# Performance work log

Hardware: AMD Instinct MI355X
Metric: run time of the kernel (lower is better)

The kernel has to match this reference:

```python
import jax, jax.numpy as jnp
import numpy as np

B, P, L, D, H = 32, 256, 64, 128, 8
DH = D // H
NP_, NL, E = B * P, B * L, B * P * L
LN_EPS = 1e-5


def setup_inputs() -> dict:
    key = jax.random.key(0)
    ks = jax.random.split(key, 32)
    def rn(i, shape, scale=0.05):
        return jax.random.normal(ks[i], shape, dtype=jnp.float32) * scale
    # uniform batch layout: graph b owns protein nodes [b*P,(b+1)*P) and ligand nodes [b*L,(b+1)*L)
    pe = (np.arange(B)[:, None] * P + np.repeat(np.arange(P), L)[None, :]).reshape(-1)
    le = (np.arange(B)[:, None] * L + np.tile(np.arange(L), P)[None, :]).reshape(-1)
    return {
        'h_protein': rn(0, (NP_, D), 1.0), 'h_ligand': rn(1, (NL, D), 1.0),
        'p_edge_idx': jnp.asarray(pe, jnp.int32), 'l_edge_idx': jnp.asarray(le, jnp.int32),
        'Wq_l': rn(2, (D, D)), 'Wk_p': rn(3, (D, D)), 'Wv_p': rn(4, (D, D)),
        'Wg_l': rn(5, (2 * D, D)), 'bg_l': jnp.zeros((D,), jnp.float32),
        'Wu_l': rn(6, (D, D)), 'bu_l': jnp.zeros((D,), jnp.float32),
        'Wq_p': rn(7, (D, D)), 'Wk_l': rn(8, (D, D)), 'Wv_l': rn(9, (D, D)),
        'Wg_p': rn(10, (2 * D, D)), 'bg_p': jnp.zeros((D,), jnp.float32),
        'Wu_p': rn(11, (D, D)), 'bu_p': jnp.zeros((D,), jnp.float32),
        'ln_p_g': jnp.ones((D,), jnp.float32), 'ln_p_b': jnp.zeros((D,), jnp.float32),
        'ln_l_g': jnp.ones((D,), jnp.float32), 'ln_l_b': jnp.zeros((D,), jnp.float32),
        'W1_p': rn(12, (D, 4 * D)), 'b1_p': jnp.zeros((4 * D,), jnp.float32),
        'W2_p': rn(13, (4 * D, D)), 'b2_p': jnp.zeros((D,), jnp.float32),
        'W1_l': rn(14, (D, 4 * D)), 'b1_l': jnp.zeros((4 * D,), jnp.float32),
        'W2_l': rn(15, (4 * D, D)), 'b2_l': jnp.zeros((D,), jnp.float32),
    }


def _layernorm(x, g, b):
    mu = jnp.mean(x, axis=-1, keepdims=True)
    var = jnp.mean(jnp.square(x - mu), axis=-1, keepdims=True)
    return (x - mu) * jax.lax.rsqrt(var + LN_EPS) * g + b


def _seg_softmax(scores, seg, n):  # scores [E,H], seg [E]
    m = jax.ops.segment_max(scores, seg, num_segments=n)
    e = jnp.exp(scores - m[seg])
    s = jax.ops.segment_sum(e, seg, num_segments=n)
    return e / s[seg]


def _side(hq, hkv, q_edge, kv_edge, nq, Wq, Wk, Wv, Wg, bg, Wu, bu):
    q = (hq @ Wq).reshape(-1, H, DH)
    k = (hkv @ Wk).reshape(-1, H, DH)
    v = (hkv @ Wv).reshape(-1, H, DH)
    scores = jnp.sum(q[q_edge] * k[kv_edge], axis=-1) / np.sqrt(DH)  # [E,H]
    att = _seg_softmax(scores, q_edge, nq)
    ctx = jax.ops.segment_sum(v[kv_edge] * att[:, :, None], q_edge, num_segments=nq)
    ctx = ctx.reshape(nq, D)
    gate = jax.nn.sigmoid(jnp.concatenate([hq, ctx], axis=1) @ Wg + bg)
    return hq + gate * (ctx @ Wu + bu)


def reference(h_protein, h_ligand, p_edge_idx, l_edge_idx,
              Wq_l, Wk_p, Wv_p, Wg_l, bg_l, Wu_l, bu_l,
              Wq_p, Wk_l, Wv_l, Wg_p, bg_p, Wu_p, bu_p,
              ln_p_g, ln_p_b, ln_l_g, ln_l_b,
              W1_p, b1_p, W2_p, b2_p, W1_l, b1_l, W2_l, b2_l):
    n_p, n_l = h_protein.shape[0], h_ligand.shape[0]
    # ligand attends to protein
    h_l_upd = _side(h_ligand, h_protein, l_edge_idx, p_edge_idx, n_l,
                    Wq_l, Wk_p, Wv_p, Wg_l, bg_l, Wu_l, bu_l)
    # protein attends to ligand
    h_p_upd = _side(h_protein, h_ligand, p_edge_idx, l_edge_idx, n_p,
                    Wq_p, Wk_l, Wv_l, Wg_p, bg_p, Wu_p, bu_p)
    # FFN blocks (dropout = identity in eval mode)
    hp = _layernorm(h_p_upd, ln_p_g, ln_p_b)
    protein_final = h_p_upd + jax.nn.relu(hp @ W1_p + b1_p) @ W2_p + b2_p
    hl = _layernorm(h_l_upd, ln_l_g, ln_l_b)
    ligand_final = h_l_upd + jax.nn.relu(hl @ W1_l + b1_l) @ W2_l + b2_l
    return (protein_final, ligand_final)
```

## Files before the change

### kernel.cpp

```cpp
#include <hip/hip_runtime.h>
#include <hip/hip_bf16.h>

typedef __bf16 bf16x8 __attribute__((ext_vector_type(8)));
typedef __bf16 bf16x4 __attribute__((ext_vector_type(4)));
typedef float  f32x4  __attribute__((ext_vector_type(4)));
typedef unsigned short u16;

#define NPROT 8192
#define NLIG  2048
#define DMODEL 128
#define NHEAD 8
#define NBATCH 32
#define PPB 256
#define LPB 64

__device__ __forceinline__ u16 f2bf(float f){
  union { float f; unsigned int u; } v; v.f = f;
  return (u16)((v.u + 0x7FFFu + ((v.u >> 16) & 1u)) >> 16);
}

__device__ __forceinline__ bf16x8 cvt8(const float* p){
  float4 a = *(const float4*)p, b = *(const float4*)(p + 4);
  bf16x8 r;
  r[0]=(__bf16)a.x; r[1]=(__bf16)a.y; r[2]=(__bf16)a.z; r[3]=(__bf16)a.w;
  r[4]=(__bf16)b.x; r[5]=(__bf16)b.y; r[6]=(__bf16)b.z; r[7]=(__bf16)b.w;
  return r;
}

struct QkvJob { const float* A; const float* Wsrc[3]; u16* outB; int N; int blockStart; };
struct TJob { const float* src; u16* dst; int M, K, tilesX, blockStart; };
struct L1Args {
  QkvJob qjobs[2];
  int nQkv;
  int nprep;
  TJob pjobs[10];
};

__global__ __launch_bounds__(256) void l1_kernel(L1Args a){
  __shared__ u16 Wl[64][136];
  __shared__ u16 Al[64][136];
  __shared__ float tile[32][33];
  int bid = (int)blockIdx.x;
  int tid = (int)threadIdx.x;
  if (bid < a.nQkv){
    int j = (bid >= a.qjobs[1].blockStart) ? 1 : 0;
    const QkvJob jb = a.qjobs[j];
    int t = bid - jb.blockStart;
    int tn = t / 6, tm = t - tn * 6;
    {
      int midx = tm >> 1;
      int cb64 = (tm & 1) * 64;
      const float* Ws = jb.Wsrc[midx];
      int kr = tid >> 2;
      int cb = (tid & 3) * 16;
      #pragma unroll
      for (int p = 0; p < 2; ++p){
        int k = p * 64 + kr;
        const float* srcp = Ws + (size_t)k * 128 + cb64 + cb;
        float4 v0 = *(const float4*)srcp,     v1 = *(const float4*)(srcp + 4);
        float4 v2 = *(const float4*)(srcp+8), v3 = *(const float4*)(srcp + 12);
        float tmp[16] = {v0.x,v0.y,v0.z,v0.w, v1.x,v1.y,v1.z,v1.w,
                         v2.x,v2.y,v2.z,v2.w, v3.x,v3.y,v3.z,v3.w};
        #pragma unroll
        for (int i = 0; i < 16; ++i) Wl[cb + i][k] = f2bf(tmp[i]);
      }
    }
    {
      const float* Asrc = jb.A + (size_t)(tn * 64) * 128;
      #pragma unroll
      for (int p = 0; p < 8; ++p){
        int idx = p * 256 + tid;
        int r = idx >> 5, c4 = (idx & 31) * 4;
        float4 v = *(const float4*)(Asrc + (size_t)r * 128 + c4);
        Al[r][c4+0] = f2bf(v.x); Al[r][c4+1] = f2bf(v.y);
        Al[r][c4+2] = f2bf(v.z); Al[r][c4+3] = f2bf(v.w);
      }
    }
    __syncthreads();
    int w = tid >> 6, l = tid & 63;
    int rloc = (w >> 1) * 32;
    int cloc = (w & 1) * 32;
    int lr = l & 15, lk = (l >> 4) * 8;
    f32x4 a00 = {0.f,0.f,0.f,0.f}, a01 = a00, a10 = a00, a11 = a00;
    #pragma unroll
    for (int kk = 0; kk < 128; kk += 32){
      bf16x8 a0 = *(const bf16x8*)&Al[rloc + lr][kk + lk];
      bf16x8 a1 = *(const bf16x8*)&Al[rloc + 16 + lr][kk + lk];
      bf16x8 b0 = *(const bf16x8*)&Wl[cloc + lr][kk + lk];
      bf16x8 b1 = *(const bf16x8*)&Wl[cloc + 16 + lr][kk + lk];
      a00 = __builtin_amdgcn_mfma_f32_16x16x32_bf16(a0, b0, a00, 0, 0, 0);
      a01 = __builtin_amdgcn_mfma_f32_16x16x32_bf16(a0, b1, a01, 0, 0, 0);
      a10 = __builtin_amdgcn_mfma_f32_16x16x32_bf16(a1, b0, a10, 0, 0, 0);
      a11 = __builtin_amdgcn_mfma_f32_16x16x32_bf16(a1, b1, a11, 0, 0, 0);
    }
    __syncthreads();
    {
      f32x4 av[2][2] = {{a00, a01}, {a10, a11}};
      int lg4 = l >> 4;
      #pragma unroll
      for (int i = 0; i < 2; ++i)
        #pragma unroll
        for (int jj = 0; jj < 2; ++jj)
          #pragma unroll
          for (int e = 0; e < 4; ++e)
            Al[rloc + i * 16 + lg4 * 4 + e][cloc + jj * 16 + lr] = f2bf(av[i][jj][e]);
    }
    __syncthreads();
    {
      int row = tid >> 2;
      int hseg = tid & 3;
      int m = tm >> 1;
      int h = (tm & 1) * 4 + hseg;
      const u16* srcl = &Al[row][hseg * 16];
      u16* dst = jb.outB + ((size_t)m * NHEAD + h) * (size_t)jb.N * 16
                         + (size_t)(tn * 64 + row) * 16;
      *(bf16x8*)dst = *(const bf16x8*)srcl;
      *(bf16x8*)(dst + 8) = *(const bf16x8*)(srcl + 8);
    }
  } else {
    int pb = bid - a.nQkv;
    int j = 0;
    while (j + 1 < a.nprep && pb >= a.pjobs[j + 1].blockStart) ++j;
    const TJob jb = a.pjobs[j];
    int t = pb - jb.blockStart;
    int tm = t % jb.tilesX, tk = t / jb.tilesX;
    int c = tid & 31, r0 = tid >> 5;
    #pragma unroll
    for (int p = 0; p < 4; ++p)
      tile[r0 + p * 8][c] = jb.src[(size_t)(tk * 32 + r0 + p * 8) * jb.M + tm * 32 + c];
    __syncthreads();
    {
      int c2 = tid >> 7;
      int lch = (tid >> 1) & 63;
      int eh = (tid & 1) * 4;
      int kl = (lch >> 4) * 8 + eh;
      int ml = c2 * 16 + (lch & 15);
      ushort4 o;
      o.x = f2bf(tile[kl + 0][ml]);
      o.y = f2bf(tile[kl + 1][ml]);
      o.z = f2bf(tile[kl + 2][ml]);
      o.w = f2bf(tile[kl + 3][ml]);
      size_t off = ((size_t)(tm * 2 + c2) * (jb.K >> 5) + tk) * 512 + lch * 8 + eh;
      *(ushort4*)&jb.dst[off] = o;
    }
  }
}

struct K2Args {
  const u16 *qkv_p, *qkv_l;
  const float *h_f[2];
  const u16 *WgT[2], *WgB[2], *WuT[2];
  const float *bg[2], *bu[2], *lng[2], *lnb[2];
  const u16 *W1T[2], *W2T[2];
  const float *b1[2], *b2[2];
  float* out[2];
};

struct K2B {
  float hu[32 * 132];
  union { float hstg[32 * 132]; u16 t[32 * 520]; } x;
};

__global__ __launch_bounds__(512) void k2_kernel(K2Args args){
  __shared__ __align__(16) union {
    struct { u16 vT[8 * 1152]; u16 P[8 * 2304]; } a;
    K2B b;
  } su;
  __shared__ __align__(16) u16 s_ctx[32 * 128];

  int bid = (int)blockIdx.x;
  int tid = (int)threadIdx.x;
  int w = tid >> 6, l = tid & 63, lr = l & 15, lg4 = l >> 4;
  int lk = lg4 * 8;

  int side, rowbase, batch, NC;
  if (bid < NLIG / 32){ side = 1; rowbase = bid * 32; batch = rowbase >> 6; NC = 4; }
  else { side = 0; rowbase = (bid - NLIG / 32) * 32; batch = rowbase >> 8; NC = 1; }

  int NRs = side == 0 ? NPROT : NLIG;
  int NRo = side == 0 ? NLIG : NPROT;
  int orowoff = side == 0 ? batch * LPB : batch * PPB;
  const u16* qbase = (side == 0 ? args.qkv_p : args.qkv_l);
  const u16* obase = (side == 0 ? args.qkv_l : args.qkv_p);
  const u16* kbase = obase + (size_t)NHEAD * NRo * 16;
  const u16* vbase = obase + (size_t)2 * NHEAD * NRo * 16;

  bf16x8 zero8;
  #pragma unroll
  for (int i = 0; i < 8; ++i) zero8[i] = (__bf16)0.f;

  u16* vTw = su.a.vT + w * 1152;
  u16* Pw  = su.a.P  + w * 2304;
  int h = w;

  {
    bf16x8 qf[2];
    #pragma unroll
    for (int qt = 0; qt < 2; ++qt)
      qf[qt] = (l < 32)
        ? *(const bf16x8*)(qbase + ((size_t)h * NRs + rowbase + qt * 16 + lr) * 16 + lk)
        : zero8;
    f32x4 Ot[2]; float mv[2], ls[2];
    #pragma unroll
    for (int qt = 0; qt < 2; ++qt){ Ot[qt] = (f32x4){0.f,0.f,0.f,0.f}; mv[qt] = -1e30f; ls[qt] = 0.f; }
    for (int c = 0; c < NC; ++c){
      {
        const u16* vs = vbase + ((size_t)h * NRo + orowoff + c * 64 + l) * 16;
        bf16x8 v0 = *(const bf16x8*)vs;
        bf16x8 v1 = *(const bf16x8*)(vs + 8);
        #pragma unroll
        for (int i = 0; i < 8; ++i){
          vTw[i * 72 + l]       = ((const u16*)&v0)[i];
          vTw[(i + 8) * 72 + l] = ((const u16*)&v1)[i];
        }
      }
      bf16x8 kf[4];
      #pragma unroll
      for (int kt = 0; kt < 4; ++kt)
        kf[kt] = (l < 32)
          ? *(const bf16x8*)(kbase + ((size_t)h * NRo + orowoff + c * 64 + kt * 16 + lr) * 16 + lk)
          : zero8;
      f32x4 sa[4][2];
      #pragma unroll
      for (int kt = 0; kt < 4; ++kt)
        #pragma unroll
        for (int qt = 0; qt < 2; ++qt)
          sa[kt][qt] = __builtin_amdgcn_mfma_f32_16x16x32_bf16(kf[kt], qf[qt], (f32x4){0.f,0.f,0.f,0.f}, 0, 0, 0);
      #pragma unroll
      for (int qt = 0; qt < 2; ++qt){
        float cm = -1e30f;
        #pragma unroll
        for (int kt = 0; kt < 4; ++kt)
          #pragma unroll
          for (int e = 0; e < 4; ++e) cm = fmaxf(cm, sa[kt][qt][e]);
        cm = fmaxf(cm, __shfl_xor(cm, 16)); cm = fmaxf(cm, __shfl_xor(cm, 32));
        float mn = fmaxf(mv[qt], cm);
        float resc = __expf((mv[qt] - mn) * 0.25f);
        mv[qt] = mn;
        float cs = 0.f;
        #pragma unroll
        for (int kt = 0; kt < 4; ++kt){
          bf16x4 pk;
          #pragma unroll
          for (int e = 0; e < 4; ++e){
            float p = __expf((sa[kt][qt][e] - mn) * 0.25f);
            cs += p; pk[e] = (__bf16)p;
          }
          *(bf16x4*)&Pw[(size_t)(qt * 16 + lr) * 72 + kt * 16 + lg4 * 4] = pk;
        }
        cs += __shfl_xor(cs, 16); cs += __shfl_xor(cs, 32);
        ls[qt] = ls[qt] * resc + cs;
        Ot[qt] = Ot[qt] * resc;
      }
      #pragma unroll
      for (int ks = 0; ks < 2; ++ks){
        bf16x8 va = *(const bf16x8*)&vTw[(size_t)lr * 72 + ks * 32 + lg4 * 8];
        #pragma unroll
        for (int qt = 0; qt < 2; ++qt){
          bf16x8 pb = *(const bf16x8*)&Pw[(size_t)(qt * 16 + lr) * 72 + ks * 32 + lg4 * 8];
          Ot[qt] = __builtin_amdgcn_mfma_f32_16x16x32_bf16(va, pb, Ot[qt], 0, 0, 0);
        }
      }
    }
    #pragma unroll
    for (int qt = 0; qt < 2; ++qt){
      float inv = 1.f / ls[qt];
      int q = qt * 16 + lr;
      int dbase = h * 16 + lg4 * 4;
      bf16x4 ov;
      #pragma unroll
      for (int e = 0; e < 4; ++e) ov[e] = (__bf16)(Ot[qt][e] * inv);
      *(bf16x4*)&s_ctx[(size_t)q * 128 + (dbase ^ ((q & 7) << 3))] = ov;
    }
  }
  __syncthreads();

  {
    const float* hsrc = args.h_f[side] + (size_t)rowbase * 128;
    #pragma unroll
    for (int p = 0; p < 2; ++p){
      int idx = p * 512 + tid;
      int r = idx >> 5, c4 = (idx & 31) * 4;
      *(float4*)&su.b.x.hstg[(size_t)r * 132 + c4] = *(const float4*)(hsrc + (size_t)r * 128 + c4);
    }
  }
  __syncthreads();

  {
    bf16x8 wg[4], wc[4], wu[4];
    {
      const u16* bgp = args.WgT[side] + (size_t)(w * 4) * 512 + l * 8;
      const u16* bcp = args.WgB[side] + (size_t)(w * 4) * 512 + l * 8;
      const u16* bup = args.WuT[side] + (size_t)(w * 4) * 512 + l * 8;
      #pragma unroll
      for (int kb = 0; kb < 4; ++kb) wg[kb] = *(const bf16x8*)(bgp + kb * 512);
      #pragma unroll
      for (int kb = 0; kb < 4; ++kb) wc[kb] = *(const bf16x8*)(bcp + kb * 512);
      #pragma unroll
      for (int kb = 0; kb < 4; ++kb) wu[kb] = *(const bf16x8*)(bup + kb * 512);
    }
    f32x4 g0 = {0.f,0.f,0.f,0.f}, g1 = g0, u0 = g0, u1 = g0;
    const float* hst = su.b.x.hstg;
    int swa = (lr & 7) << 3;
    #pragma unroll
    for (int kb = 0; kb < 4; ++kb){
      int kk = kb * 32;
      bf16x8 ah0 = cvt8(hst + (size_t)lr * 132 + kk);
      bf16x8 ah1 = cvt8(hst + (size_t)(16 + lr) * 132 + kk);
      bf16x8 ac0 = *(const bf16x8*)&s_ctx[(size_t)lr * 128 + ((kk + lk) ^ swa)];
      bf16x8 ac1 = *(const bf16x8*)&s_ctx[(size_t)(16 + lr) * 128 + ((kk + lk) ^ swa)];
      g0 = __builtin_amdgcn_mfma_f32_16x16x32_bf16(ah0, wg[kb], g0, 0, 0, 0);
      g1 = __builtin_amdgcn_mfma_f32_16x16x32_bf16(ah1, wg[kb], g1, 0, 0, 0);
      g0 = __builtin_amdgcn_mfma_f32_16x16x32_bf16(ac0, wc[kb], g0, 0, 0, 0);
      g1 = __builtin_amdgcn_mfma_f32_16x16x32_bf16(ac1, wc[kb], g1, 0, 0, 0);
      u0 = __builtin_amdgcn_mfma_f32_16x16x32_bf16(ac0, wu[kb], u0, 0, 0, 0);
      u1 = __builtin_amdgcn_mfma_f32_16x16x32_bf16(ac1, wu[kb], u1, 0, 0, 0);
    }
    int col = w * 16 + lr;
    float bgc = args.bg[side][col];
    float buc = args.bu[side][col];
    #pragma unroll
    for (int i = 0; i < 2; ++i){
      f32x4 gv4 = i ? g1 : g0;
      f32x4 uv4 = i ? u1 : u0;
      #pragma unroll
      for (int e = 0; e < 4; ++e){
        int row = i * 16 + lg4 * 4 + e;
        float gv = gv4[e] + bgc;
        float uv = uv4[e] + buc;
        float hv = hst[(size_t)row * 132 + col];
        float sg = 1.f / (1.f + __expf(-gv));
        su.b.hu[(size_t)row * 132 + col] = hv + sg * uv;
      }
    }
  }
  __syncthreads();

  {
    int r = tid >> 4;
    int sub = tid & 15;
    float x[8];
    #pragma unroll
    for (int i = 0; i < 2; ++i){
      float4 v4 = *(const float4*)&su.b.hu[(size_t)r * 132 + sub * 8 + i * 4];
      x[i*4+0] = v4.x; x[i*4+1] = v4.y; x[i*4+2] = v4.z; x[i*4+3] = v4.w;
    }
    float s = 0.f;
    #pragma unroll
    for (int i = 0; i < 8; ++i) s += x[i];
    s += __shfl_xor(s, 1); s += __shfl_xor(s, 2); s += __shfl_xor(s, 4); s += __shfl_xor(s, 8);
    float mu = s * (1.f / 128.f);
    float vv = 0.f;
    #pragma unroll
    for (int i = 0; i < 8; ++i){ float d = x[i] - mu; vv += d * d; }
    vv += __shfl_xor(vv, 1); vv += __shfl_xor(vv, 2); vv += __shfl_xor(vv, 4); vv += __shfl_xor(vv, 8);
    float rs = rsqrtf(vv * (1.f / 128.f) + 1e-5f);
    const float* lg2 = args.lng[side];
    const float* lb = args.lnb[side];
    int sw = (r & 7) << 3;
    #pragma unroll
    for (int i = 0; i < 8; ++i){
      int col = sub * 8 + i;
      s_ctx[(size_t)r * 128 + (col ^ sw)] = f2bf((x[i] - mu) * rs * lg2[col] + lb[col]);
    }
  }
  __syncthreads();

  {
    bf16x8 w1f[16];
    {
      const u16* b1p = args.W1T[side] + (size_t)(w * 16) * 512 + l * 8;
      #pragma unroll
      for (int q = 0; q < 16; ++q) w1f[q] = *(const bf16x8*)(b1p + q * 512);
    }
    f32x4 acc[2][4];
    #pragma unroll
    for (int i = 0; i < 2; ++i)
      #pragma unroll
      for (int jj = 0; jj < 4; ++jj) acc[i][jj] = (f32x4){0.f,0.f,0.f,0.f};
    int sw0 = (lr & 7) << 3;
    #pragma unroll
    for (int kb = 0; kb < 4; ++kb){
      int kk = kb * 32;
      bf16x8 a0 = *(const bf16x8*)&s_ctx[(size_t)lr * 128 + ((kk + lk) ^ sw0)];
      bf16x8 a1 = *(const bf16x8*)&s_ctx[(size_t)(16 + lr) * 128 + ((kk + lk) ^ sw0)];
      #pragma unroll
      for (int jj = 0; jj < 4; ++jj){
        acc[0][jj] = __builtin_amdgcn_mfma_f32_16x16x32_bf16(a0, w1f[jj * 4 + kb], acc[0][jj], 0, 0, 0);
        acc[1][jj] = __builtin_amdgcn_mfma_f32_16x16x32_bf16(a1, w1f[jj * 4 + kb], acc[1][jj], 0, 0, 0);
      }
    }
    const float* b1v = args.b1[side];
    u16* t_flat = su.b.x.t;
    #pragma unroll
    for (int i = 0; i < 2; ++i)
      #pragma unroll
      for (int jj = 0; jj < 4; ++jj)
        #pragma unroll
        for (int e = 0; e < 4; ++e){
          int row = i * 16 + lg4 * 4 + e;
          int col = w * 64 + jj * 16 + lr;
          float v = fmaxf(acc[i][jj][e] + b1v[col], 0.f);
          t_flat[(size_t)row * 520 + (col ^ ((row & 7) << 3))] = f2bf(v);
        }
  }
  __syncthreads();

  {
    bf16x8 w2f[16];
    {
      const u16* b2p = args.W2T[side] + (size_t)(w * 16) * 512 + l * 8;
      #pragma unroll
      for (int q = 0; q < 16; ++q) w2f[q] = *(const bf16x8*)(b2p + q * 512);
    }
    f32x4 o[2][2];
    #pragma unroll
    for (int i = 0; i < 2; ++i)
      #pragma unroll
      for (int p = 0; p < 2; ++p) o[i][p] = (f32x4){0.f,0.f,0.f,0.f};
    const u16* t_flat = su.b.x.t;
    int sw0 = (lr & 7) << 3;
    #pragma unroll
    for (int kb = 0; kb < 16; kb += 2){
      int kk = kb * 32;
      bf16x8 a0e = *(const bf16x8*)&t_flat[(size_t)lr * 520 + ((kk + lk) ^ sw0)];
      bf16x8 a1e = *(const bf16x8*)&t_flat[(size_t)(16 + lr) * 520 + ((kk + lk) ^ sw0)];
      bf16x8 a0o = *(const bf16x8*)&t_flat[(size_t)lr * 520 + ((kk + 32 + lk) ^ sw0)];
      bf16x8 a1o = *(const bf16x8*)&t_flat[(size_t)(16 + lr) * 520 + ((kk + 32 + lk) ^ sw0)];
      o[0][0] = __builtin_amdgcn_mfma_f32_16x16x32_bf16(a0e, w2f[kb],     o[0][0], 0, 0, 0);
      o[1][0] = __builtin_amdgcn_mfma_f32_16x16x32_bf16(a1e, w2f[kb],     o[1][0], 0, 0, 0);
      o[0][1] = __builtin_amdgcn_mfma_f32_16x16x32_bf16(a0o, w2f[kb + 1], o[0][1], 0, 0, 0);
      o[1][1] = __builtin_amdgcn_mfma_f32_16x16x32_bf16(a1o, w2f[kb + 1], o[1][1], 0, 0, 0);
    }
    const float* b2v = args.b2[side];
    float* outp = args.out[side];
    int col = w * 16 + lr;
    float b2c = b2v[col];
    #pragma unroll
    for (int i = 0; i < 2; ++i){
      #pragma unroll
      for (int e = 0; e < 4; ++e){
        int row = i * 16 + lg4 * 4 + e;
        float val = o[i][0][e] + o[i][1][e] + b2c + su.b.hu[(size_t)row * 132 + col];
        outp[(size_t)(rowbase + row) * 128 + col] = val;
      }
    }
  }
}

extern "C" void kernel_launch(void* const* d_in, const int* in_sizes, int n_in,
                              void* d_out, int out_size, void* d_ws, size_t ws_size,
                              hipStream_t stream) {
  (void)in_sizes; (void)n_in; (void)out_size; (void)ws_size;
  const float* h_p  = (const float*)d_in[0];
  const float* h_l  = (const float*)d_in[1];
  const float* Wq_l = (const float*)d_in[4];
  const float* Wk_p = (const float*)d_in[5];
  const float* Wv_p = (const float*)d_in[6];
  const float* Wg_l = (const float*)d_in[7];
  const float* bg_l = (const float*)d_in[8];
  const float* Wu_l = (const float*)d_in[9];
  const float* bu_l = (const float*)d_in[10];
  const float* Wq_p = (const float*)d_in[11];
  const float* Wk_l = (const float*)d_in[12];
  const float* Wv_l = (const float*)d_in[13];
  const float* Wg_p = (const float*)d_in[14];
  const float* bg_p = (const float*)d_in[15];
  const float* Wu_p = (const float*)d_in[16];
  const float* bu_p = (const float*)d_in[17];
  const float* ln_p_g = (const float*)d_in[18];
  const float* ln_p_b = (const float*)d_in[19];
  const float* ln_l_g = (const float*)d_in[20];
  const float* ln_l_b = (const float*)d_in[21];
  const float* W1_p = (const float*)d_in[22];
  const float* b1_p = (const float*)d_in[23];
  const float* W2_p = (const float*)d_in[24];
  const float* b2_p = (const float*)d_in[25];
  const float* W1_l = (const float*)d_in[26];
  const float* b1_l = (const float*)d_in[27];
  const float* W2_l = (const float*)d_in[28];
  const float* b2_l = (const float*)d_in[29];
  float* out = (float*)d_out;

  char* ws = (char*)d_ws;
  size_t off = 0;
  auto alloc = [&](size_t bytes) -> void* {
    void* p = ws + off; off += (bytes + 255) & ~(size_t)255; return p;
  };
  u16* WgT_p_T = (u16*)alloc((size_t)128 * 128 * 2);
  u16* WgB_p_T = (u16*)alloc((size_t)128 * 128 * 2);
  u16* Wu_p_T  = (u16*)alloc((size_t)128 * 128 * 2);
  u16* WgT_l_T = (u16*)alloc((size_t)128 * 128 * 2);
  u16* WgB_l_T = (u16*)alloc((size_t)128 * 128 * 2);
  u16* Wu_l_T  = (u16*)alloc((size_t)128 * 128 * 2);
  u16* W1_p_T  = (u16*)alloc((size_t)512 * 128 * 2);
  u16* W1_l_T  = (u16*)alloc((size_t)512 * 128 * 2);
  u16* W2_p_T  = (u16*)alloc((size_t)128 * 512 * 2);
  u16* W2_l_T  = (u16*)alloc((size_t)128 * 512 * 2);
  u16* qkv_p   = (u16*)alloc((size_t)NPROT * 384 * 2);
  u16* qkv_l   = (u16*)alloc((size_t)NLIG  * 384 * 2);

  {
    L1Args a;
    a.qjobs[0] = { h_p, {Wq_p, Wk_p, Wv_p}, qkv_p, NPROT, 0 };
    a.qjobs[1] = { h_l, {Wq_l, Wk_l, Wv_l}, qkv_l, NLIG, (NPROT / 64) * 6 };
    a.nQkv = (NPROT / 64) * 6 + (NLIG / 64) * 6;
    int pbs = 0;
    int pi = 0;
    auto addT = [&](const float* s, u16* d, int K, int M){
      a.pjobs[pi].src = s; a.pjobs[pi].dst = d; a.pjobs[pi].M = M; a.pjobs[pi].K = K;
      a.pjobs[pi].tilesX = M / 32; a.pjobs[pi].blockStart = pbs;
      pbs += (K / 32) * (M / 32); ++pi;
    };
    addT(Wg_l,             WgT_l_T, 128, 128);
    addT(Wg_l + 128 * 128, WgB_l_T, 128, 128);
    addT(Wu_l,             Wu_l_T,  128, 128);
    addT(Wg_p,             WgT_p_T, 128, 128);
    addT(Wg_p + 128 * 128, WgB_p_T, 128, 128);
    addT(Wu_p,             Wu_p_T,  128, 128);
    addT(W1_p, W1_p_T, 128, 512);
    addT(W2_p, W2_p_T, 512, 128);
    addT(W1_l, W1_l_T, 128, 512);
    addT(W2_l, W2_l_T, 512, 128);
    a.nprep = pi;
    l1_kernel<<<dim3(a.nQkv + pbs), dim3(256), 0, stream>>>(a);
  }

  {
    K2Args k;
    k.qkv_p = qkv_p; k.qkv_l = qkv_l;
    k.h_f[0] = h_p; k.h_f[1] = h_l;
    k.WgT[0] = WgT_p_T; k.WgT[1] = WgT_l_T;
    k.WgB[0] = WgB_p_T; k.WgB[1] = WgB_l_T;
    k.WuT[0] = Wu_p_T;  k.WuT[1] = Wu_l_T;
    k.bg[0] = bg_p; k.bg[1] = bg_l;
    k.bu[0] = bu_p; k.bu[1] = bu_l;
    k.lng[0] = ln_p_g; k.lng[1] = ln_l_g;
    k.lnb[0] = ln_p_b; k.lnb[1] = ln_l_b;
    k.W1T[0] = W1_p_T; k.W1T[1] = W1_l_T;
    k.W2T[0] = W2_p_T; k.W2T[1] = W2_l_T;
    k.b1[0] = b1_p; k.b1[1] = b1_l;
    k.b2[0] = b2_p; k.b2[1] = b2_l;
    k.out[0] = out; k.out[1] = out + (size_t)NPROT * DMODEL;
    k2_kernel<<<dim3(NLIG / 32 + NPROT / 32), dim3(512), 0, stream>>>(k);
  }
}
```

Measured before the change: 39.68 us.

## Prefetch K/V, residual rows and FFN weights early; remap l1 block order

The attention loop now double-buffers K/V chunk loads in registers, fetching the next chunk while computing the current one, and skips the rescale on the first chunk. The residual input rows and the gate/update/W1/W2 weight fragments are loaded one stage ahead of their use, so global latency can hide behind earlier MFMA work and barriers. The l1 kernel also permutes block IDs across 8 groups, which looks like an XCD-aware remap. This raises register pressure, which may lower occupancy, and the hardcoded 164 in the remap assumes a specific grid size.

```diff
diff --git a/kernel.cpp b/kernel.cpp
--- a/kernel.cpp
+++ b/kernel.cpp
@@ -41,6 +41,7 @@
   __shared__ u16 Al[64][136];
   __shared__ float tile[32][33];
   int bid = (int)blockIdx.x;
+  bid = (bid & 7) * 164 + (bid >> 3);
   int tid = (int)threadIdx.x;
   if (bid < a.nQkv){
     int j = (bid >= a.qjobs[1].blockStart) ? 1 : 0;
@@ -193,6 +194,18 @@
   u16* Pw  = su.a.P  + w * 2304;
   int h = w;
 
+  float4 hreg0, hreg1;
+  {
+    const float* hsrc = args.h_f[side] + (size_t)rowbase * 128;
+    int i1 = 512 + tid;
+    hreg0 = *(const float4*)(hsrc + (size_t)(tid >> 5) * 128 + (tid & 31) * 4);
+    hreg1 = *(const float4*)(hsrc + (size_t)(i1 >> 5) * 128 + (i1 & 31) * 4);
+  }
+
+  bf16x8 wg[4], wc[4], wu[4];
+  bf16x8 w1f[16];
+  bf16x8 w2f[16];
+
   {
     bf16x8 qf[2];
     #pragma unroll
@@ -200,26 +213,39 @@
       qf[qt] = (l < 32)
         ? *(const bf16x8*)(qbase + ((size_t)h * NRs + rowbase + qt * 16 + lr) * 16 + lk)
         : zero8;
+    bf16x8 vr0, vr1, kn[4];
+    {
+      const u16* vs = vbase + ((size_t)h * NRo + orowoff + l) * 16;
+      vr0 = *(const bf16x8*)vs;
+      vr1 = *(const bf16x8*)(vs + 8);
+      #pragma unroll
+      for (int kt = 0; kt < 4; ++kt)
+        kn[kt] = (l < 32)
+          ? *(const bf16x8*)(kbase + ((size_t)h * NRo + orowoff + kt * 16 + lr) * 16 + lk)
+          : zero8;
+    }
     f32x4 Ot[2]; float mv[2], ls[2];
     #pragma unroll
     for (int qt = 0; qt < 2; ++qt){ Ot[qt] = (f32x4){0.f,0.f,0.f,0.f}; mv[qt] = -1e30f; ls[qt] = 0.f; }
     for (int c = 0; c < NC; ++c){
-      {
-        const u16* vs = vbase + ((size_t)h * NRo + orowoff + c * 64 + l) * 16;
-        bf16x8 v0 = *(const bf16x8*)vs;
-        bf16x8 v1 = *(const bf16x8*)(vs + 8);
-        #pragma unroll
-        for (int i = 0; i < 8; ++i){
-          vTw[i * 72 + l]       = ((const u16*)&v0)[i];
-          vTw[(i + 8) * 72 + l] = ((const u16*)&v1)[i];
-        }
+      #pragma unroll
+      for (int i = 0; i < 8; ++i){
+        vTw[i * 72 + l]       = ((const u16*)&vr0)[i];
+        vTw[(i + 8) * 72 + l] = ((const u16*)&vr1)[i];
       }
       bf16x8 kf[4];
       #pragma unroll
-      for (int kt = 0; kt < 4; ++kt)
-        kf[kt] = (l < 32)
-          ? *(const bf16x8*)(kbase + ((size_t)h * NRo + orowoff + c * 64 + kt * 16 + lr) * 16 + lk)
-          : zero8;
+      for (int kt = 0; kt < 4; ++kt) kf[kt] = kn[kt];
+      if (c + 1 < NC){
+        const u16* vs = vbase + ((size_t)h * NRo + orowoff + (c + 1) * 64 + l) * 16;
+        vr0 = *(const bf16x8*)vs;
+        vr1 = *(const bf16x8*)(vs + 8);
+        #pragma unroll
+        for (int kt = 0; kt < 4; ++kt)
+          kn[kt] = (l < 32)
+            ? *(const bf16x8*)(kbase + ((size_t)h * NRo + orowoff + (c + 1) * 64 + kt * 16 + lr) * 16 + lk)
+            : zero8;
+      }
       f32x4 sa[4][2];
       #pragma unroll
       for (int kt = 0; kt < 4; ++kt)
@@ -234,8 +260,9 @@
           #pragma unroll
           for (int e = 0; e < 4; ++e) cm = fmaxf(cm, sa[kt][qt][e]);
         cm = fmaxf(cm, __shfl_xor(cm, 16)); cm = fmaxf(cm, __shfl_xor(cm, 32));
-        float mn = fmaxf(mv[qt], cm);
-        float resc = __expf((mv[qt] - mn) * 0.25f);
+        float mn, resc;
+        if (c == 0){ mn = cm; resc = 0.f; }
+        else { mn = fmaxf(mv[qt], cm); resc = __expf((mv[qt] - mn) * 0.25f); }
         mv[qt] = mn;
         float cs = 0.f;
         #pragma unroll
@@ -262,6 +289,17 @@
         }
       }
     }
+    {
+      const u16* bgp = args.WgT[side] + (size_t)(w * 4) * 512 + l * 8;
+      const u16* bcp = args.WgB[side] + (size_t)(w * 4) * 512 + l * 8;
+      const u16* bup = args.WuT[side] + (size_t)(w * 4) * 512 + l * 8;
+      #pragma unroll
+      for (int kb = 0; kb < 4; ++kb) wg[kb] = *(const bf16x8*)(bgp + kb * 512);
+      #pragma unroll
+      for (int kb = 0; kb < 4; ++kb) wc[kb] = *(const bf16x8*)(bcp + kb * 512);
+      #pragma unroll
+      for (int kb = 0; kb < 4; ++kb) wu[kb] = *(const bf16x8*)(bup + kb * 512);
+    }
     #pragma unroll
     for (int qt = 0; qt < 2; ++qt){
       float inv = 1.f / ls[qt];
@@ -276,29 +314,13 @@
   __syncthreads();
 
   {
-    const float* hsrc = args.h_f[side] + (size_t)rowbase * 128;
-    #pragma unroll
-    for (int p = 0; p < 2; ++p){
-      int idx = p * 512 + tid;
-      int r = idx >> 5, c4 = (idx & 31) * 4;
-      *(float4*)&su.b.x.hstg[(size_t)r * 132 + c4] = *(const float4*)(hsrc + (size_t)r * 128 + c4);
-    }
+    int i1 = 512 + tid;
+    *(float4*)&su.b.x.hstg[(size_t)(tid >> 5) * 132 + (tid & 31) * 4] = hreg0;
+    *(float4*)&su.b.x.hstg[(size_t)(i1 >> 5) * 132 + (i1 & 31) * 4] = hreg1;
   }
   __syncthreads();
 
   {
-    bf16x8 wg[4], wc[4], wu[4];
-    {
-      const u16* bgp = args.WgT[side] + (size_t)(w * 4) * 512 + l * 8;
-      const u16* bcp = args.WgB[side] + (size_t)(w * 4) * 512 + l * 8;
-      const u16* bup = args.WuT[side] + (size_t)(w * 4) * 512 + l * 8;
-      #pragma unroll
-      for (int kb = 0; kb < 4; ++kb) wg[kb] = *(const bf16x8*)(bgp + kb * 512);
-      #pragma unroll
-      for (int kb = 0; kb < 4; ++kb) wc[kb] = *(const bf16x8*)(bcp + kb * 512);
-      #pragma unroll
-      for (int kb = 0; kb < 4; ++kb) wu[kb] = *(const bf16x8*)(bup + kb * 512);
-    }
     f32x4 g0 = {0.f,0.f,0.f,0.f}, g1 = g0, u0 = g0, u1 = g0;
     const float* hst = su.b.x.hstg;
     int swa = (lr & 7) << 3;
@@ -316,9 +338,15 @@
       u0 = __builtin_amdgcn_mfma_f32_16x16x32_bf16(ac0, wu[kb], u0, 0, 0, 0);
       u1 = __builtin_amdgcn_mfma_f32_16x16x32_bf16(ac1, wu[kb], u1, 0, 0, 0);
     }
+    {
+      const u16* b1p = args.W1T[side] + (size_t)(w * 16) * 512 + l * 8;
+      #pragma unroll
+      for (int q = 0; q < 16; ++q) w1f[q] = *(const bf16x8*)(b1p + q * 512);
+    }
     int col = w * 16 + lr;
     float bgc = args.bg[side][col];
     float buc = args.bu[side][col];
+    const float* hst2 = su.b.x.hstg;
     #pragma unroll
     for (int i = 0; i < 2; ++i){
       f32x4 gv4 = i ? g1 : g0;
@@ -328,7 +356,7 @@
         int row = i * 16 + lg4 * 4 + e;
         float gv = gv4[e] + bgc;
         float uv = uv4[e] + buc;
-        float hv = hst[(size_t)row * 132 + col];
+        float hv = hst2[(size_t)row * 132 + col];
         float sg = 1.f / (1.f + __expf(-gv));
         su.b.hu[(size_t)row * 132 + col] = hv + sg * uv;
       }
@@ -367,12 +395,6 @@
   __syncthreads();
 
   {
-    bf16x8 w1f[16];
-    {
-      const u16* b1p = args.W1T[side] + (size_t)(w * 16) * 512 + l * 8;
-      #pragma unroll
-      for (int q = 0; q < 16; ++q) w1f[q] = *(const bf16x8*)(b1p + q * 512);
-    }
     f32x4 acc[2][4];
     #pragma unroll
     for (int i = 0; i < 2; ++i)
@@ -389,6 +411,11 @@
         acc[0][jj] = __builtin_amdgcn_mfma_f32_16x16x32_bf16(a0, w1f[jj * 4 + kb], acc[0][jj], 0, 0, 0);
         acc[1][jj] = __builtin_amdgcn_mfma_f32_16x16x32_bf16(a1, w1f[jj * 4 + kb], acc[1][jj], 0, 0, 0);
       }
+    }
+    {
+      const u16* b2p = args.W2T[side] + (size_t)(w * 16) * 512 + l * 8;
+      #pragma unroll
+      for (int q = 0; q < 16; ++q) w2f[q] = *(const bf16x8*)(b2p + q * 512);
     }
     const float* b1v = args.b1[side];
     u16* t_flat = su.b.x.t;
@@ -407,12 +434,6 @@
   __syncthreads();
 
   {
-    bf16x8 w2f[16];
-    {
-      const u16* b2p = args.W2T[side] + (size_t)(w * 16) * 512 + l * 8;
-      #pragma unroll
-      for (int q = 0; q < 16; ++q) w2f[q] = *(const bf16x8*)(b2p + q * 512);
-    }
     f32x4 o[2][2];
     #pragma unroll
     for (int i = 0; i < 2; ++i)
```

Measured after the change: 43.98 us. +10.8%, slower.

## Widen QKV projection tiles to 192 columns with 512-thread blocks

Applied to the files above, without the earlier changes.

The QKV projection blocks now compute a 64x192 output tile with 8 waves, where each wave does a 32x48 sub-tile, instead of a 64x64 tile with 4 waves. This cuts the QKV block count threefold, so each input row tile is loaded and converted to bf16 two times rather than six. The 192x136 weight LDS buffer is reused for output staging with a 200-element row stride. The weight transpose prep blocks now run with half their threads idle, and the larger LDS footprint and block size may reduce occupancy.

```diff
diff --git a/kernel.cpp b/kernel.cpp
--- a/kernel.cpp
+++ b/kernel.cpp
@@ -36,8 +36,8 @@
   TJob pjobs[10];
 };
 
-__global__ __launch_bounds__(256) void l1_kernel(L1Args a){
-  __shared__ u16 Wl[64][136];
+__global__ __launch_bounds__(512) void l1_kernel(L1Args a){
+  __shared__ u16 Wl[192 * 136];
   __shared__ u16 Al[64][136];
   __shared__ float tile[32][33];
   int bid = (int)blockIdx.x;
@@ -46,30 +46,27 @@
     int j = (bid >= a.qjobs[1].blockStart) ? 1 : 0;
     const QkvJob jb = a.qjobs[j];
     int t = bid - jb.blockStart;
-    int tn = t / 6, tm = t - tn * 6;
-    {
-      int midx = tm >> 1;
-      int cb64 = (tm & 1) * 64;
-      const float* Ws = jb.Wsrc[midx];
+    int tn = t >> 1, tm2 = t & 1;
+    {
       int kr = tid >> 2;
-      int cb = (tid & 3) * 16;
-      #pragma unroll
-      for (int p = 0; p < 2; ++p){
-        int k = p * 64 + kr;
-        const float* srcp = Ws + (size_t)k * 128 + cb64 + cb;
-        float4 v0 = *(const float4*)srcp,     v1 = *(const float4*)(srcp + 4);
-        float4 v2 = *(const float4*)(srcp+8), v3 = *(const float4*)(srcp + 12);
-        float tmp[16] = {v0.x,v0.y,v0.z,v0.w, v1.x,v1.y,v1.z,v1.w,
-                         v2.x,v2.y,v2.z,v2.w, v3.x,v3.y,v3.z,v3.w};
-        #pragma unroll
-        for (int i = 0; i < 16; ++i) Wl[cb + i][k] = f2bf(tmp[i]);
+      int ci = (tid & 3) * 4;
+      #pragma unroll
+      for (int cg = 0; cg < 12; ++cg){
+        int gcol = tm2 * 192 + cg * 16;
+        const float* Ws = jb.Wsrc[gcol >> 7];
+        int mcol = gcol & 127;
+        float4 v = *(const float4*)(Ws + (size_t)kr * 128 + mcol + ci);
+        Wl[(cg * 16 + ci + 0) * 136 + kr] = f2bf(v.x);
+        Wl[(cg * 16 + ci + 1) * 136 + kr] = f2bf(v.y);
+        Wl[(cg * 16 + ci + 2) * 136 + kr] = f2bf(v.z);
+        Wl[(cg * 16 + ci + 3) * 136 + kr] = f2bf(v.w);
       }
     }
     {
       const float* Asrc = jb.A + (size_t)(tn * 64) * 128;
       #pragma unroll
-      for (int p = 0; p < 8; ++p){
-        int idx = p * 256 + tid;
+      for (int p = 0; p < 4; ++p){
+        int idx = p * 512 + tid;
         int r = idx >> 5, c4 = (idx & 31) * 4;
         float4 v = *(const float4*)(Asrc + (size_t)r * 128 + c4);
         Al[r][c4+0] = f2bf(v.x); Al[r][c4+1] = f2bf(v.y);
@@ -78,44 +75,50 @@
     }
     __syncthreads();
     int w = tid >> 6, l = tid & 63;
-    int rloc = (w >> 1) * 32;
-    int cloc = (w & 1) * 32;
+    int rloc = (w >> 2) * 32;
+    int cloc = (w & 3) * 48;
     int lr = l & 15, lk = (l >> 4) * 8;
-    f32x4 a00 = {0.f,0.f,0.f,0.f}, a01 = a00, a10 = a00, a11 = a00;
+    f32x4 acc[2][3];
+    #pragma unroll
+    for (int i = 0; i < 2; ++i)
+      #pragma unroll
+      for (int f = 0; f < 3; ++f) acc[i][f] = (f32x4){0.f,0.f,0.f,0.f};
     #pragma unroll
     for (int kk = 0; kk < 128; kk += 32){
       bf16x8 a0 = *(const bf16x8*)&Al[rloc + lr][kk + lk];
       bf16x8 a1 = *(const bf16x8*)&Al[rloc + 16 + lr][kk + lk];
-      bf16x8 b0 = *(const bf16x8*)&Wl[cloc + lr][kk + lk];
-      bf16x8 b1 = *(const bf16x8*)&Wl[cloc + 16 + lr][kk + lk];
-      a00 = __builtin_amdgcn_mfma_f32_16x16x32_bf16(a0, b0, a00, 0, 0, 0);
-      a01 = __builtin_amdgcn_mfma_f32_16x16x32_bf16(a0, b1, a01, 0, 0, 0);
-      a10 = __builtin_amdgcn_mfma_f32_16x16x32_bf16(a1, b0, a10, 0, 0, 0);
-      a11 = __builtin_amdgcn_mfma_f32_16x16x32_bf16(a1, b1, a11, 0, 0, 0);
+      #pragma unroll
+      for (int f = 0; f < 3; ++f){
+        bf16x8 b = *(const bf16x8*)&Wl[(size_t)(cloc + f * 16 + lr) * 136 + kk + lk];
+        acc[0][f] = __builtin_amdgcn_mfma_f32_16x16x32_bf16(a0, b, acc[0][f], 0, 0, 0);
+        acc[1][f] = __builtin_amdgcn_mfma_f32_16x16x32_bf16(a1, b, acc[1][f], 0, 0, 0);
+      }
     }
     __syncthreads();
     {
-      f32x4 av[2][2] = {{a00, a01}, {a10, a11}};
       int lg4 = l >> 4;
       #pragma unroll
       for (int i = 0; i < 2; ++i)
         #pragma unroll
-        for (int jj = 0; jj < 2; ++jj)
+        for (int f = 0; f < 3; ++f)
           #pragma unroll
           for (int e = 0; e < 4; ++e)
-            Al[rloc + i * 16 + lg4 * 4 + e][cloc + jj * 16 + lr] = f2bf(av[i][jj][e]);
+            Wl[(size_t)(rloc + i * 16 + lg4 * 4 + e) * 200 + cloc + f * 16 + lr] = f2bf(acc[i][f][e]);
     }
     __syncthreads();
     {
-      int row = tid >> 2;
-      int hseg = tid & 3;
-      int m = tm >> 1;
-      int h = (tm & 1) * 4 + hseg;
-      const u16* srcl = &Al[row][hseg * 16];
-      u16* dst = jb.outB + ((size_t)m * NHEAD + h) * (size_t)jb.N * 16
-                         + (size_t)(tn * 64 + row) * 16;
-      *(bf16x8*)dst = *(const bf16x8*)srcl;
-      *(bf16x8*)(dst + 8) = *(const bf16x8*)(srcl + 8);
+      for (int ii = tid; ii < 768; ii += 512){
+        int row = ii / 12;
+        int sg  = ii - row * 12;
+        int gcol = tm2 * 192 + sg * 16;
+        int m = gcol >> 7;
+        int h = (gcol >> 4) & 7;
+        const u16* srcl = &Wl[(size_t)row * 200 + sg * 16];
+        u16* dst = jb.outB + ((size_t)m * NHEAD + h) * (size_t)jb.N * 16
+                           + (size_t)(tn * 64 + row) * 16;
+        *(bf16x8*)dst = *(const bf16x8*)srcl;
+        *(bf16x8*)(dst + 8) = *(const bf16x8*)(srcl + 8);
+      }
     }
   } else {
     int pb = bid - a.nQkv;
@@ -124,12 +127,14 @@
     const TJob jb = a.pjobs[j];
     int t = pb - jb.blockStart;
     int tm = t % jb.tilesX, tk = t / jb.tilesX;
-    int c = tid & 31, r0 = tid >> 5;
-    #pragma unroll
-    for (int p = 0; p < 4; ++p)
-      tile[r0 + p * 8][c] = jb.src[(size_t)(tk * 32 + r0 + p * 8) * jb.M + tm * 32 + c];
+    int c = tid & 31, r0 = (tid >> 5) & 7;
+    if (tid < 256){
+      #pragma unroll
+      for (int p = 0; p < 4; ++p)
+        tile[r0 + p * 8][c] = jb.src[(size_t)(tk * 32 + r0 + p * 8) * jb.M + tm * 32 + c];
+    }
     __syncthreads();
-    {
+    if (tid < 256){
       int c2 = tid >> 7;
       int lch = (tid >> 1) & 63;
       int eh = (tid & 1) * 4;
@@ -503,8 +508,8 @@
   {
     L1Args a;
     a.qjobs[0] = { h_p, {Wq_p, Wk_p, Wv_p}, qkv_p, NPROT, 0 };
-    a.qjobs[1] = { h_l, {Wq_l, Wk_l, Wv_l}, qkv_l, NLIG, (NPROT / 64) * 6 };
-    a.nQkv = (NPROT / 64) * 6 + (NLIG / 64) * 6;
+    a.qjobs[1] = { h_l, {Wq_l, Wk_l, Wv_l}, qkv_l, NLIG, (NPROT / 64) * 2 };
+    a.nQkv = (NPROT / 64) * 2 + (NLIG / 64) * 2;
     int pbs = 0;
     int pi = 0;
     auto addT = [&](const float* s, u16* d, int K, int M){
@@ -523,7 +528,7 @@
     addT(W1_l, W1_l_T, 128, 512);
     addT(W2_l, W2_l_T, 512, 128);
     a.nprep = pi;
-    l1_kernel<<<dim3(a.nQkv + pbs), dim3(256), 0, stream>>>(a);
+    l1_kernel<<<dim3(a.nQkv + pbs), dim3(512), 0, stream>>>(a);
   }
 
   {
```

New measurement: 41.11 us. 1.04x slower.
